# Performance work log

Hardware: AMD Instinct MI355X
Metric: run time of the kernel (lower is better)

The kernel has to match this reference:

```python
import jax, jax.numpy as jnp
import numpy as np

B, S, L, H, C = 16, 2048, 256, 768, 512

def setup_inputs() -> dict:
    key = jax.random.key(0)
    ks = jax.random.split(key, 9)
    sc = 1.0 / np.sqrt(H)
    return {
        "input_hidden_states": jax.random.normal(ks[0], (B, S, H), jnp.float32),
        "label_hidden_states": jax.random.normal(ks[1], (L, H), jnp.float32),
        "Wi": jax.random.normal(ks[2], (C, H), jnp.float32) * sc,
        "bi": jnp.zeros((C,), jnp.float32),
        "Wl": jax.random.normal(ks[3], (C, H), jnp.float32) * sc,
        "bl": jnp.zeros((C,), jnp.float32),
        "Wia": jax.random.normal(ks[4], (C, H), jnp.float32) * sc,
        "bia": jnp.zeros((C,), jnp.float32),
        "Wla": jax.random.normal(ks[5], (C, H), jnp.float32) * sc,
        "bla": jnp.zeros((C,), jnp.float32),
        "context": jax.random.uniform(ks[6], (C,), jnp.float32),
        "Wp": jax.random.normal(ks[7], (H, C), jnp.float32) * (1.0 / np.sqrt(C)),
    }

def reference(input_hidden_states, label_hidden_states, Wi, bi, Wl, bl,
              Wia, bia, Wla, bla, context, Wp):
    # Dropout is identity in eval mode.
    x = input_hidden_states            # [B,S,H]
    lab = label_hidden_states          # [L,H] (original repeats over batch; math is identical)
    input_trans = jax.nn.sigmoid(jnp.einsum('bsh,ch->bsc', x, Wi) + bi)      # [B,S,C]
    label_trans = jax.nn.sigmoid(lab @ Wl.T + bl)                            # [L,C]
    input_attn = jax.nn.sigmoid(jnp.einsum('bsh,ch->bsc', x, Wia) + bia)    # [B,S,C]
    label_attn = jax.nn.sigmoid(lab @ Wla.T + bla)                          # [L,C]
    # attn logits: (context * input_attn) @ label_attn^T  -> [B,S,L]
    logits = jnp.einsum('bsc,lc->bsl', input_attn * context, label_attn)
    attn = jax.nn.softmax(logits, axis=-1)                                   # [B,S,L]
    # trilinear reduction: sum_{s,l} input_trans[b,s,c] * attn[b,s,l] * label_trans[l,c]
    weighted = jnp.einsum('bsl,lc->bsc', attn, label_trans)                  # [B,S,C]
    fusion = jnp.sum(input_trans * weighted, axis=1)                         # [B,C]
    return fusion @ Wp.T                                                     # [B,H]
```

## Files before the change

### kernel.cpp

```cpp
#include <hip/hip_runtime.h>

#define H_DIM 768
#define C_DIM 512
#define L_DIM 256
#define S_DIM 2048
#define B_DIM 16

#define IA_STRIDE 520
#define ATTN_STRIDE 264

typedef __attribute__((ext_vector_type(8))) short short8;
typedef __attribute__((ext_vector_type(4))) float f32x4;
typedef __attribute__((ext_vector_type(2))) __fp16 half2v;

#define MFMA_F16(a, b, c) __builtin_amdgcn_mfma_f32_16x16x32_f16((a), (b), (c), 0, 0, 0)

__device__ __forceinline__ unsigned short f2h(float f) {
    _Float16 h = (_Float16)f;
    return __builtin_bit_cast(unsigned short, h);
}
__device__ __forceinline__ float h2f(unsigned short u) {
    _Float16 h = __builtin_bit_cast(_Float16, u);
    return (float)h;
}
__device__ __forceinline__ float sigmoid_f(float x) { return 1.0f / (1.0f + __expf(-x)); }

__device__ __forceinline__ short8 cvt8(const float* p) {
    const float4* q = (const float4*)(const void*)p;
    float4 u = q[0], v = q[1];
    half2v h0 = __builtin_amdgcn_cvt_pkrtz(u.x, u.y);
    half2v h1 = __builtin_amdgcn_cvt_pkrtz(u.z, u.w);
    half2v h2 = __builtin_amdgcn_cvt_pkrtz(v.x, v.y);
    half2v h3 = __builtin_amdgcn_cvt_pkrtz(v.z, v.w);
    int4 pk = { __builtin_bit_cast(int, h0), __builtin_bit_cast(int, h1),
                __builtin_bit_cast(int, h2), __builtin_bit_cast(int, h3) };
    return __builtin_bit_cast(short8, pk);
}


__global__ __launch_bounds__(256) void prep_w(
    const float* __restrict__ Wi, const float* __restrict__ Wia,
    const float* __restrict__ Wl, const float* __restrict__ Wla,
    unsigned short* __restrict__ Wi_f, unsigned short* __restrict__ Wia_f,
    unsigned short* __restrict__ Wl_f, unsigned short* __restrict__ Wla_f)
{
    const int tid = blockIdx.x * 256 + threadIdx.x;
    const int m   = tid / 49152;
    const int idx = tid - m * 49152;
    const int ct   = idx / 1536;
    const int rem  = idx - ct * 1536;
    const int kt   = rem >> 6;
    const int lane = rem & 63;
    const int row  = ct * 16 + (lane & 15);
    const int kcol = kt * 32 + (lane >> 4) * 8;
    const float* src = (m == 0 ? Wi : (m == 1 ? Wia : (m == 2 ? Wl : Wla)));
    unsigned short* dst = (m == 0 ? Wi_f : (m == 1 ? Wia_f : (m == 2 ? Wl_f : Wla_f)));
    short8 v = cvt8(src + (size_t)row * H_DIM + kcol);
    const int frag = ((ct >> 3) * 24 + kt) * 8 + (ct & 7);
    *(short8*)(void*)(dst + ((size_t)frag * 64 + lane) * 8) = v;
}

__global__ __launch_bounds__(256) void prep_x(
    const float* __restrict__ x, unsigned short* __restrict__ x_f)
{
    const int tid = blockIdx.x * 256 + threadIdx.x;
    const int mt  = tid / 1536;
    const int rem = tid - mt * 1536;
    const int kt  = rem >> 6;
    const int lane = rem & 63;
    const int row = mt * 16 + (lane & 15);
    const int col = kt * 32 + (lane >> 4) * 8;
    short8 v = cvt8(x + (size_t)row * H_DIM + col);
    *(short8*)(void*)(x_f + ((size_t)(mt * 24 + kt) * 64 + lane) * 8) = v;
}

__global__ __launch_bounds__(256) void label_mfma(
    const float* __restrict__ lab,
    const unsigned short* __restrict__ Wl_f,  const float* __restrict__ bl,
    const unsigned short* __restrict__ Wla_f, const float* __restrict__ bla,
    const float* __restrict__ ctx,
    unsigned short* __restrict__ la_f,
    unsigned short* __restrict__ lt_f)
{
    const int tid  = threadIdx.x;
    const int wave = tid >> 6;
    const int lane = tid & 63;
    const int quad = lane >> 4;
    const int c16  = lane & 15;
    const int ct2  = blockIdx.x & 7;
    const int mh   = blockIdx.x >> 3;
    const int ct   = ct2 * 4 + wave;
    const int n0   = ct * 16;
    const int l0   = mh * 32;

    const f32x4 z4 = {0.f, 0.f, 0.f, 0.f};
    f32x4 a1[2], a2[2];
#pragma unroll
    for (int mt = 0; mt < 2; ++mt) { a1[mt] = z4; a2[mt] = z4; }

    const float* lb = lab + (size_t)(l0 + c16) * H_DIM + quad * 8;
    const short8* wl8  = (const short8*)(const void*)Wl_f  + ((size_t)(ct >> 3) * 24 * 8 + (ct & 7)) * 64 + lane;
    const short8* wla8 = (const short8*)(const void*)Wla_f + ((size_t)(ct >> 3) * 24 * 8 + (ct & 7)) * 64 + lane;
    for (int kt = 0; kt < 24; ++kt) {
        short8 b1 = wl8[kt * 8 * 64];
        short8 b2 = wla8[kt * 8 * 64];
#pragma unroll
        for (int mt = 0; mt < 2; ++mt) {
            short8 a = cvt8(lb + mt * 16 * H_DIM + kt * 32);
            a1[mt] = MFMA_F16(a, b1, a1[mt]);
            a2[mt] = MFMA_F16(a, b2, a2[mt]);
        }
    }
    const int c = n0 + c16;
    const float blv = bl[c], blav = bla[c], cv = ctx[c];
#pragma unroll
    for (int mt = 0; mt < 2; ++mt)
#pragma unroll
        for (int r = 0; r < 4; ++r) {
            const int l = l0 + mt * 16 + quad * 4 + r;
            const float ltv = sigmoid_f(a1[mt][r] + blv);
            const float lav = sigmoid_f(a2[mt][r] + blav) * cv;
            {
                const int ctc = c >> 4, ktl = l >> 5;
                const int frag = ((ctc >> 3) * 8 + ktl) * 8 + (ctc & 7);
                const int ln = (c & 15) | (((l >> 3) & 3) << 4);
                lt_f[((size_t)frag * 64 + ln) * 8 + (l & 7)] = f2h(ltv);
            }
            {
                const int lt = l >> 4, ktc = c >> 5;
                const int frag = ((lt >> 2) * 16 + ktc) * 4 + (lt & 3);
                const int ln = (l & 15) | (((c >> 3) & 3) << 4);
                la_f[((size_t)frag * 64 + ln) * 8 + (c & 7)] = f2h(lav);
            }
        }
}

template<bool XF>
__global__ __launch_bounds__(256, 4) void fused_main(
    const unsigned short* __restrict__ x_f,
    const float* __restrict__ x,
    const float* __restrict__ bi,
    const float* __restrict__ bia,
    const unsigned short* __restrict__ Wi_f,
    const unsigned short* __restrict__ Wia_f,
    const unsigned short* __restrict__ lt_f,
    const unsigned short* __restrict__ la_f,
    float* __restrict__ fusion)
{
    __shared__ unsigned short lds_buf[32 * IA_STRIDE];
    __shared__ float rowscratch[4 * 32];
    __shared__ float inv_lds[32];

    const int tid  = threadIdx.x;
    const int wave = tid >> 6;
    const int lane = tid & 63;
    const int quad = lane >> 4;
    const int c16  = lane & 15;

    const int row0 = blockIdx.x * 32;
    const int b    = row0 >> 11;

    const f32x4 z4 = {0.f, 0.f, 0.f, 0.f};
    const int n0 = wave * 128;

    const float*  xb  = x + (size_t)(row0 + c16) * H_DIM + quad * 8;
    const short8* xf8 = (const short8*)(const void*)x_f + ((size_t)blockIdx.x * 2 * 24) * 64 + lane;

    {
        f32x4 acc[2][8];
#pragma unroll
        for (int mt = 0; mt < 2; ++mt)
#pragma unroll
            for (int nt = 0; nt < 8; ++nt) acc[mt][nt] = z4;
        const short8* wa8 = (const short8*)(const void*)Wia_f + (size_t)wave * 192 * 64 + lane;
        for (int kt = 0; kt < 24; ++kt) {
            short8 a0, a1;
            if constexpr (XF) { a0 = xf8[kt * 64]; a1 = xf8[(24 + kt) * 64]; }
            else { a0 = cvt8(xb + kt * 32); a1 = cvt8(xb + 16 * H_DIM + kt * 32); }
#pragma unroll
            for (int nt = 0; nt < 8; ++nt) {
                short8 ba = wa8[(kt * 8 + nt) * 64];
                acc[0][nt] = MFMA_F16(a0, ba, acc[0][nt]);
                acc[1][nt] = MFMA_F16(a1, ba, acc[1][nt]);
            }
        }
#pragma unroll
        for (int nt = 0; nt < 8; ++nt) {
            const int col = n0 + nt * 16 + c16;
            const float bv = bia[col];
#pragma unroll
            for (int mt = 0; mt < 2; ++mt)
#pragma unroll
                for (int r = 0; r < 4; ++r) {
                    const int row = mt * 16 + quad * 4 + r;
                    lds_buf[row * IA_STRIDE + col] = f2h(sigmoid_f(acc[mt][nt][r] + bv));
                }
        }
    }
    __syncthreads();

    const int n0l = wave * 64;
    f32x4 accl[2][4];
#pragma unroll
    for (int mt = 0; mt < 2; ++mt)
#pragma unroll
        for (int nt = 0; nt < 4; ++nt) accl[mt][nt] = z4;
    {
        const unsigned short* ab = lds_buf + c16 * IA_STRIDE + quad * 8;
        const short8* la8 = (const short8*)(const void*)la_f + (size_t)wave * 64 * 64 + lane;
        for (int kt = 0; kt < 16; ++kt) {
            const int kk = kt * 32;
            short8 a0 = *(const short8*)(const void*)(ab + kk);
            short8 a1 = *(const short8*)(const void*)(ab + 16 * IA_STRIDE + kk);
#pragma unroll
            for (int nt = 0; nt < 4; ++nt) {
                short8 bfr = la8[(kt * 4 + nt) * 64];
                accl[0][nt] = MFMA_F16(a0, bfr, accl[0][nt]);
                accl[1][nt] = MFMA_F16(a1, bfr, accl[1][nt]);
            }
        }
    }
    __syncthreads();

    float rmax[2][4];
#pragma unroll
    for (int mt = 0; mt < 2; ++mt)
#pragma unroll
        for (int r = 0; r < 4; ++r) {
            float m = accl[mt][0][r];
#pragma unroll
            for (int nt = 1; nt < 4; ++nt) m = fmaxf(m, accl[mt][nt][r]);
#pragma unroll
            for (int off = 1; off < 16; off <<= 1) m = fmaxf(m, __shfl_xor(m, off, 64));
            rmax[mt][r] = m;
        }
    if (c16 == 0) {
#pragma unroll
        for (int mt = 0; mt < 2; ++mt)
#pragma unroll
            for (int r = 0; r < 4; ++r)
                rowscratch[wave * 32 + mt * 16 + quad * 4 + r] = rmax[mt][r];
    }
    __syncthreads();
    float rsum[2][4];
#pragma unroll
    for (int mt = 0; mt < 2; ++mt)
#pragma unroll
        for (int r = 0; r < 4; ++r) {
            const int row = mt * 16 + quad * 4 + r;
            float gm = rowscratch[row];
#pragma unroll
            for (int w = 1; w < 4; ++w) gm = fmaxf(gm, rowscratch[w * 32 + row]);
            float s = 0.f;
#pragma unroll
            for (int nt = 0; nt < 4; ++nt) {
                float e = __expf(accl[mt][nt][r] - gm);
                accl[mt][nt][r] = e;
                s += e;
            }
#pragma unroll
            for (int off = 1; off < 16; off <<= 1) s += __shfl_xor(s, off, 64);
            rsum[mt][r] = s;
        }
    __syncthreads();
    if (c16 == 0) {
#pragma unroll
        for (int mt = 0; mt < 2; ++mt)
#pragma unroll
            for (int r = 0; r < 4; ++r)
                rowscratch[wave * 32 + mt * 16 + quad * 4 + r] = rsum[mt][r];
    }
    __syncthreads();
#pragma unroll
    for (int mt = 0; mt < 2; ++mt)
#pragma unroll
        for (int r = 0; r < 4; ++r) {
            const int row = mt * 16 + quad * 4 + r;
            const float st = rowscratch[row] + rowscratch[32 + row]
                           + rowscratch[64 + row] + rowscratch[96 + row];
            if (wave == 0 && c16 == 0) inv_lds[row] = 1.0f / st;
#pragma unroll
            for (int nt = 0; nt < 4; ++nt)
                lds_buf[row * ATTN_STRIDE + n0l + nt * 16 + c16] = f2h(accl[mt][nt][r]);
        }
    __syncthreads();

    f32x4 accw[2][8];
#pragma unroll
    for (int mt = 0; mt < 2; ++mt)
#pragma unroll
        for (int nt = 0; nt < 8; ++nt) accw[mt][nt] = z4;
    {
        const unsigned short* ab = lds_buf + c16 * ATTN_STRIDE + quad * 8;
        const short8* lt8 = (const short8*)(const void*)lt_f + (size_t)wave * 64 * 64 + lane;
        for (int kt = 0; kt < 8; ++kt) {
            const int kk = kt * 32;
            short8 a0 = *(const short8*)(const void*)(ab + kk);
            short8 a1 = *(const short8*)(const void*)(ab + 16 * ATTN_STRIDE + kk);
#pragma unroll
            for (int nt = 0; nt < 8; ++nt) {
                short8 bfr = lt8[(kt * 8 + nt) * 64];
                accw[0][nt] = MFMA_F16(a0, bfr, accw[0][nt]);
                accw[1][nt] = MFMA_F16(a1, bfr, accw[1][nt]);
            }
        }
    }
    __syncthreads();

    {
        float invr[2][4];
#pragma unroll
        for (int mt = 0; mt < 2; ++mt)
#pragma unroll
            for (int r = 0; r < 4; ++r) invr[mt][r] = inv_lds[mt * 16 + quad * 4 + r];
#pragma unroll
        for (int nt = 0; nt < 8; ++nt) {
            const int col = n0 + nt * 16 + c16;
#pragma unroll
            for (int mt = 0; mt < 2; ++mt)
#pragma unroll
                for (int r = 0; r < 4; ++r) {
                    const int row = mt * 16 + quad * 4 + r;
                    lds_buf[row * IA_STRIDE + col] = f2h(accw[mt][nt][r] * invr[mt][r]);
                }
        }
    }

    {
        f32x4 acc[2][8];
#pragma unroll
        for (int mt = 0; mt < 2; ++mt)
#pragma unroll
            for (int nt = 0; nt < 8; ++nt) acc[mt][nt] = z4;
        const short8* wi8 = (const short8*)(const void*)Wi_f + (size_t)wave * 192 * 64 + lane;
        for (int kt = 0; kt < 24; ++kt) {
            short8 a0, a1;
            if constexpr (XF) { a0 = xf8[kt * 64]; a1 = xf8[(24 + kt) * 64]; }
            else { a0 = cvt8(xb + kt * 32); a1 = cvt8(xb + 16 * H_DIM + kt * 32); }
#pragma unroll
            for (int nt = 0; nt < 8; ++nt) {
                short8 bw = wi8[(kt * 8 + nt) * 64];
                acc[0][nt] = MFMA_F16(a0, bw, acc[0][nt]);
                acc[1][nt] = MFMA_F16(a1, bw, acc[1][nt]);
            }
        }
#pragma unroll
        for (int nt = 0; nt < 8; ++nt) {
            const int col = n0 + nt * 16 + c16;
            const float bv = bi[col];
            float s = 0.f;
#pragma unroll
            for (int mt = 0; mt < 2; ++mt)
#pragma unroll
                for (int r = 0; r < 4; ++r) {
                    const int row = mt * 16 + quad * 4 + r;
                    s += h2f(lds_buf[row * IA_STRIDE + col]) * sigmoid_f(acc[mt][nt][r] + bv);
                }
            s += __shfl_xor(s, 16, 64);
            s += __shfl_xor(s, 32, 64);
            if (lane < 16) atomicAdd(&fusion[b * C_DIM + col], s);
        }
    }
}

__global__ __launch_bounds__(256) void out_kernel(
    const float* __restrict__ fusion,
    const float* __restrict__ Wp,
    float* __restrict__ out)
{
    const int idx = blockIdx.x * 256 + threadIdx.x;
    const int R   = idx >> 3;
    const int sub = idx & 7;
    const int bb  = R / H_DIM;
    const int h   = R - bb * H_DIM;
    const float* wp = Wp + (size_t)h * C_DIM;
    const float* f  = fusion + bb * C_DIM;
    float s = 0.f;
#pragma unroll
    for (int j = 0; j < 16; ++j) {
        const int c = j * 32 + sub * 4;
        float4 wv = *(const float4*)(const void*)(wp + c);
        float4 fv = *(const float4*)(const void*)(f + c);
        s += fv.x * wv.x + fv.y * wv.y + fv.z * wv.z + fv.w * wv.w;
    }
    s += __shfl_xor(s, 1, 64);
    s += __shfl_xor(s, 2, 64);
    s += __shfl_xor(s, 4, 64);
    if (sub == 0) out[R] = s;
}

extern "C" void kernel_launch(void* const* d_in, const int* in_sizes, int n_in,
                              void* d_out, int out_size, void* d_ws, size_t ws_size,
                              hipStream_t stream)
{
    const float* x    = (const float*)d_in[0];
    const float* lab  = (const float*)d_in[1];
    const float* Wi   = (const float*)d_in[2];
    const float* bi   = (const float*)d_in[3];
    const float* Wl   = (const float*)d_in[4];
    const float* bl   = (const float*)d_in[5];
    const float* Wia  = (const float*)d_in[6];
    const float* bia  = (const float*)d_in[7];
    const float* Wla  = (const float*)d_in[8];
    const float* bla  = (const float*)d_in[9];
    const float* ctx  = (const float*)d_in[10];
    const float* Wp   = (const float*)d_in[11];

    char* ws = (char*)d_ws;
    unsigned short* Wi_f  = (unsigned short*)(ws);
    unsigned short* Wia_f = (unsigned short*)(ws + 786432);
    unsigned short* Wl_f  = (unsigned short*)(ws + 1572864);
    unsigned short* Wla_f = (unsigned short*)(ws + 2359296);
    unsigned short* la_f  = (unsigned short*)(ws + 3145728);
    unsigned short* lt_f  = (unsigned short*)(ws + 3407872);
    float* fusion         = (float*)(ws + 3670016);
    unsigned short* x_f   = (unsigned short*)(ws + 3702784);
    const size_t NEED_XF  = 3702784 + (size_t)32768 * 768 * 2;

    (void)hipMemsetAsync(fusion, 0, B_DIM * C_DIM * sizeof(float), stream);
    prep_w<<<768, 256, 0, stream>>>(Wi, Wia, Wl, Wla, Wi_f, Wia_f, Wl_f, Wla_f);
    label_mfma<<<64, 256, 0, stream>>>(lab, Wl_f, bl, Wla_f, bla, ctx, la_f, lt_f);
    if (ws_size >= NEED_XF) {
        prep_x<<<12288, 256, 0, stream>>>(x, x_f);
        fused_main<true><<<(B_DIM * S_DIM) / 32, 256, 0, stream>>>(
            x_f, x, bi, bia, Wi_f, Wia_f, lt_f, la_f, fusion);
    } else {
        fused_main<false><<<(B_DIM * S_DIM) / 32, 256, 0, stream>>>(
            nullptr, x, bi, bia, Wi_f, Wia_f, lt_f, la_f, fusion);
    }
    out_kernel<<<384, 256, 0, stream>>>(fusion, Wp, (float*)d_out);
}
```

Measured before the change: 332.4 us.

## Enlarge fused block to 64 rows with 8 waves and 4x4 MFMA tiles

The fused main kernel now handles 64 rows per block with 512 threads (8 waves). Each wave owns a 4x4 grid of MFMA tiles instead of 2x8, which cuts how often each weight fragment is loaded per row and gives a squarer register tile. The fragment layouts for x, the weights and the label tensors are regrouped to match, and the label kernel is split into smaller tiles. The x and weight conversion kernels and the fusion zeroing are merged into one launch, replacing the memset and one kernel launch. The cost is a larger LDS footprint, more accumulator registers per wave and a cross-wave softmax reduction over 8 waves, all of which may reduce occupancy.

```diff
diff --git a/kernel.cpp b/kernel.cpp
--- a/kernel.cpp
+++ b/kernel.cpp
@@ -38,40 +38,48 @@
 }
 
 
-__global__ __launch_bounds__(256) void prep_w(
+__global__ __launch_bounds__(256) void prep_all(
+    const float* __restrict__ x,
     const float* __restrict__ Wi, const float* __restrict__ Wia,
     const float* __restrict__ Wl, const float* __restrict__ Wla,
+    unsigned short* __restrict__ x_f,
     unsigned short* __restrict__ Wi_f, unsigned short* __restrict__ Wia_f,
-    unsigned short* __restrict__ Wl_f, unsigned short* __restrict__ Wla_f)
+    unsigned short* __restrict__ Wl_f, unsigned short* __restrict__ Wla_f,
+    float* __restrict__ fusion, int nx)
 {
-    const int tid = blockIdx.x * 256 + threadIdx.x;
-    const int m   = tid / 49152;
-    const int idx = tid - m * 49152;
-    const int ct   = idx / 1536;
-    const int rem  = idx - ct * 1536;
-    const int kt   = rem >> 6;
-    const int lane = rem & 63;
-    const int row  = ct * 16 + (lane & 15);
-    const int kcol = kt * 32 + (lane >> 4) * 8;
-    const float* src = (m == 0 ? Wi : (m == 1 ? Wia : (m == 2 ? Wl : Wla)));
-    unsigned short* dst = (m == 0 ? Wi_f : (m == 1 ? Wia_f : (m == 2 ? Wl_f : Wla_f)));
-    short8 v = cvt8(src + (size_t)row * H_DIM + kcol);
-    const int frag = ((ct >> 3) * 24 + kt) * 8 + (ct & 7);
-    *(short8*)(void*)(dst + ((size_t)frag * 64 + lane) * 8) = v;
-}
-
-__global__ __launch_bounds__(256) void prep_x(
-    const float* __restrict__ x, unsigned short* __restrict__ x_f)
-{
-    const int tid = blockIdx.x * 256 + threadIdx.x;
-    const int mt  = tid / 1536;
-    const int rem = tid - mt * 1536;
-    const int kt  = rem >> 6;
-    const int lane = rem & 63;
-    const int row = mt * 16 + (lane & 15);
-    const int col = kt * 32 + (lane >> 4) * 8;
-    short8 v = cvt8(x + (size_t)row * H_DIM + col);
-    *(short8*)(void*)(x_f + ((size_t)(mt * 24 + kt) * 64 + lane) * 8) = v;
+    int bid = blockIdx.x;
+    if (bid < nx) {
+        const int tid = bid * 256 + threadIdx.x;
+        const int mt  = tid / 1536;
+        const int rem = tid - mt * 1536;
+        const int kt  = rem >> 6;
+        const int lane = rem & 63;
+        const int row = mt * 16 + (lane & 15);
+        const int col = kt * 32 + (lane >> 4) * 8;
+        short8 v = cvt8(x + (size_t)row * H_DIM + col);
+        const int frag = ((mt >> 2) * 24 + kt) * 4 + (mt & 3);
+        *(short8*)(void*)(x_f + ((size_t)frag * 64 + lane) * 8) = v;
+        return;
+    }
+    bid -= nx;
+    if (bid < 768) {
+        const int tid = bid * 256 + threadIdx.x;
+        const int m   = tid / 49152;
+        const int idx = tid - m * 49152;
+        const int ct   = idx / 1536;
+        const int rem  = idx - ct * 1536;
+        const int kt   = rem >> 6;
+        const int lane = rem & 63;
+        const int row  = ct * 16 + (lane & 15);
+        const int kcol = kt * 32 + (lane >> 4) * 8;
+        const float* src = (m == 0 ? Wi : (m == 1 ? Wia : (m == 2 ? Wl : Wla)));
+        unsigned short* dst = (m == 0 ? Wi_f : (m == 1 ? Wia_f : (m == 2 ? Wl_f : Wla_f)));
+        short8 v = cvt8(src + (size_t)row * H_DIM + kcol);
+        const int frag = ((ct >> 2) * 24 + kt) * 4 + (ct & 3);
+        *(short8*)(void*)(dst + ((size_t)frag * 64 + lane) * 8) = v;
+        return;
+    }
+    for (int i = threadIdx.x; i < B_DIM * C_DIM; i += 256) fusion[i] = 0.f;
 }
 
 __global__ __launch_bounds__(256) void label_mfma(
@@ -89,54 +97,46 @@
     const int c16  = lane & 15;
     const int ct2  = blockIdx.x & 7;
     const int mh   = blockIdx.x >> 3;
-    const int ct   = ct2 * 4 + wave;
-    const int n0   = ct * 16;
-    const int l0   = mh * 32;
+    const int n0   = (ct2 * 4 + wave) * 16;
+    const int l0   = mh * 16;
 
     const f32x4 z4 = {0.f, 0.f, 0.f, 0.f};
-    f32x4 a1[2], a2[2];
-#pragma unroll
-    for (int mt = 0; mt < 2; ++mt) { a1[mt] = z4; a2[mt] = z4; }
+    f32x4 a1 = z4, a2 = z4;
 
     const float* lb = lab + (size_t)(l0 + c16) * H_DIM + quad * 8;
-    const short8* wl8  = (const short8*)(const void*)Wl_f  + ((size_t)(ct >> 3) * 24 * 8 + (ct & 7)) * 64 + lane;
-    const short8* wla8 = (const short8*)(const void*)Wla_f + ((size_t)(ct >> 3) * 24 * 8 + (ct & 7)) * 64 + lane;
+    const short8* wl8  = (const short8*)(const void*)Wl_f  + ((size_t)ct2 * 96 + wave) * 64 + lane;
+    const short8* wla8 = (const short8*)(const void*)Wla_f + ((size_t)ct2 * 96 + wave) * 64 + lane;
     for (int kt = 0; kt < 24; ++kt) {
-        short8 b1 = wl8[kt * 8 * 64];
-        short8 b2 = wla8[kt * 8 * 64];
-#pragma unroll
-        for (int mt = 0; mt < 2; ++mt) {
-            short8 a = cvt8(lb + mt * 16 * H_DIM + kt * 32);
-            a1[mt] = MFMA_F16(a, b1, a1[mt]);
-            a2[mt] = MFMA_F16(a, b2, a2[mt]);
-        }
+        short8 b1 = wl8[kt * 4 * 64];
+        short8 b2 = wla8[kt * 4 * 64];
+        short8 a  = cvt8(lb + kt * 32);
+        a1 = MFMA_F16(a, b1, a1);
+        a2 = MFMA_F16(a, b2, a2);
     }
     const int c = n0 + c16;
     const float blv = bl[c], blav = bla[c], cv = ctx[c];
 #pragma unroll
-    for (int mt = 0; mt < 2; ++mt)
-#pragma unroll
-        for (int r = 0; r < 4; ++r) {
-            const int l = l0 + mt * 16 + quad * 4 + r;
-            const float ltv = sigmoid_f(a1[mt][r] + blv);
-            const float lav = sigmoid_f(a2[mt][r] + blav) * cv;
-            {
-                const int ctc = c >> 4, ktl = l >> 5;
-                const int frag = ((ctc >> 3) * 8 + ktl) * 8 + (ctc & 7);
-                const int ln = (c & 15) | (((l >> 3) & 3) << 4);
-                lt_f[((size_t)frag * 64 + ln) * 8 + (l & 7)] = f2h(ltv);
-            }
-            {
-                const int lt = l >> 4, ktc = c >> 5;
-                const int frag = ((lt >> 2) * 16 + ktc) * 4 + (lt & 3);
-                const int ln = (l & 15) | (((c >> 3) & 3) << 4);
-                la_f[((size_t)frag * 64 + ln) * 8 + (c & 7)] = f2h(lav);
-            }
-        }
+    for (int r = 0; r < 4; ++r) {
+        const int l = l0 + quad * 4 + r;
+        const float ltv = sigmoid_f(a1[r] + blv);
+        const float lav = sigmoid_f(a2[r] + blav) * cv;
+        {
+            const int ctc = c >> 4, ktl = l >> 5;
+            const int frag = ((ctc >> 2) * 8 + ktl) * 4 + (ctc & 3);
+            const int ln = (c & 15) | (((l >> 3) & 3) << 4);
+            lt_f[((size_t)frag * 64 + ln) * 8 + (l & 7)] = f2h(ltv);
+        }
+        {
+            const int lt = l >> 4, ktc = c >> 5;
+            const int frag = ((lt >> 1) * 16 + ktc) * 2 + (lt & 1);
+            const int ln = (l & 15) | (((c >> 3) & 3) << 4);
+            la_f[((size_t)frag * 64 + ln) * 8 + (c & 7)] = f2h(lav);
+        }
+    }
 }
 
 template<bool XF>
-__global__ __launch_bounds__(256, 4) void fused_main(
+__global__ __launch_bounds__(512, 4) void fused_main(
     const unsigned short* __restrict__ x_f,
     const float* __restrict__ x,
     const float* __restrict__ bi,
@@ -147,9 +147,9 @@
     const unsigned short* __restrict__ la_f,
     float* __restrict__ fusion)
 {
-    __shared__ unsigned short lds_buf[32 * IA_STRIDE];
-    __shared__ float rowscratch[4 * 32];
-    __shared__ float inv_lds[32];
+    __shared__ unsigned short lds_buf[64 * IA_STRIDE];
+    __shared__ float rowscratch[8 * 64];
+    __shared__ float inv_lds[64];
 
     const int tid  = threadIdx.x;
     const int wave = tid >> 6;
@@ -157,204 +157,208 @@
     const int quad = lane >> 4;
     const int c16  = lane & 15;
 
-    const int row0 = blockIdx.x * 32;
+    const int row0 = blockIdx.x * 64;
     const int b    = row0 >> 11;
 
     const f32x4 z4 = {0.f, 0.f, 0.f, 0.f};
-    const int n0 = wave * 128;
+    const int n0  = wave * 64;
+    const int n0l = wave * 32;
 
     const float*  xb  = x + (size_t)(row0 + c16) * H_DIM + quad * 8;
-    const short8* xf8 = (const short8*)(const void*)x_f + ((size_t)blockIdx.x * 2 * 24) * 64 + lane;
+    const short8* xf8 = (const short8*)(const void*)x_f + ((size_t)blockIdx.x * 96) * 64 + lane;
 
     {
-        f32x4 acc[2][8];
-#pragma unroll
-        for (int mt = 0; mt < 2; ++mt)
-#pragma unroll
-            for (int nt = 0; nt < 8; ++nt) acc[mt][nt] = z4;
-        const short8* wa8 = (const short8*)(const void*)Wia_f + (size_t)wave * 192 * 64 + lane;
+        f32x4 acc[4][4];
+#pragma unroll
+        for (int m = 0; m < 4; ++m)
+#pragma unroll
+            for (int p = 0; p < 4; ++p) acc[m][p] = z4;
+        const short8* wa8 = (const short8*)(const void*)Wia_f + ((size_t)wave * 96) * 64 + lane;
         for (int kt = 0; kt < 24; ++kt) {
-            short8 a0, a1;
-            if constexpr (XF) { a0 = xf8[kt * 64]; a1 = xf8[(24 + kt) * 64]; }
-            else { a0 = cvt8(xb + kt * 32); a1 = cvt8(xb + 16 * H_DIM + kt * 32); }
-#pragma unroll
-            for (int nt = 0; nt < 8; ++nt) {
-                short8 ba = wa8[(kt * 8 + nt) * 64];
-                acc[0][nt] = MFMA_F16(a0, ba, acc[0][nt]);
-                acc[1][nt] = MFMA_F16(a1, ba, acc[1][nt]);
+            short8 a[4], bw[4];
+#pragma unroll
+            for (int m = 0; m < 4; ++m) {
+                if constexpr (XF) a[m] = xf8[(kt * 4 + m) * 64];
+                else a[m] = cvt8(xb + m * 16 * H_DIM + kt * 32);
             }
-        }
-#pragma unroll
-        for (int nt = 0; nt < 8; ++nt) {
-            const int col = n0 + nt * 16 + c16;
+#pragma unroll
+            for (int p = 0; p < 4; ++p) bw[p] = wa8[(kt * 4 + p) * 64];
+#pragma unroll
+            for (int m = 0; m < 4; ++m)
+#pragma unroll
+                for (int p = 0; p < 4; ++p) acc[m][p] = MFMA_F16(a[m], bw[p], acc[m][p]);
+        }
+#pragma unroll
+        for (int p = 0; p < 4; ++p) {
+            const int col = n0 + p * 16 + c16;
             const float bv = bia[col];
 #pragma unroll
-            for (int mt = 0; mt < 2; ++mt)
+            for (int m = 0; m < 4; ++m)
 #pragma unroll
                 for (int r = 0; r < 4; ++r) {
-                    const int row = mt * 16 + quad * 4 + r;
-                    lds_buf[row * IA_STRIDE + col] = f2h(sigmoid_f(acc[mt][nt][r] + bv));
+                    const int row = m * 16 + quad * 4 + r;
+                    lds_buf[row * IA_STRIDE + col] = f2h(sigmoid_f(acc[m][p][r] + bv));
                 }
         }
     }
     __syncthreads();
 
-    const int n0l = wave * 64;
-    f32x4 accl[2][4];
-#pragma unroll
-    for (int mt = 0; mt < 2; ++mt)
-#pragma unroll
-        for (int nt = 0; nt < 4; ++nt) accl[mt][nt] = z4;
+    f32x4 accl[4][2];
+#pragma unroll
+    for (int m = 0; m < 4; ++m) { accl[m][0] = z4; accl[m][1] = z4; }
     {
         const unsigned short* ab = lds_buf + c16 * IA_STRIDE + quad * 8;
-        const short8* la8 = (const short8*)(const void*)la_f + (size_t)wave * 64 * 64 + lane;
+        const short8* la8 = (const short8*)(const void*)la_f + ((size_t)wave * 32) * 64 + lane;
         for (int kt = 0; kt < 16; ++kt) {
             const int kk = kt * 32;
-            short8 a0 = *(const short8*)(const void*)(ab + kk);
-            short8 a1 = *(const short8*)(const void*)(ab + 16 * IA_STRIDE + kk);
-#pragma unroll
-            for (int nt = 0; nt < 4; ++nt) {
-                short8 bfr = la8[(kt * 4 + nt) * 64];
-                accl[0][nt] = MFMA_F16(a0, bfr, accl[0][nt]);
-                accl[1][nt] = MFMA_F16(a1, bfr, accl[1][nt]);
+            short8 a[4], bq[2];
+#pragma unroll
+            for (int m = 0; m < 4; ++m)
+                a[m] = *(const short8*)(const void*)(ab + m * 16 * IA_STRIDE + kk);
+            bq[0] = la8[(kt * 2 + 0) * 64];
+            bq[1] = la8[(kt * 2 + 1) * 64];
+#pragma unroll
+            for (int m = 0; m < 4; ++m) {
+                accl[m][0] = MFMA_F16(a[m], bq[0], accl[m][0]);
+                accl[m][1] = MFMA_F16(a[m], bq[1], accl[m][1]);
             }
         }
     }
     __syncthreads();
 
-    float rmax[2][4];
-#pragma unroll
-    for (int mt = 0; mt < 2; ++mt)
+    float rmax[4][4];
+#pragma unroll
+    for (int m = 0; m < 4; ++m)
 #pragma unroll
         for (int r = 0; r < 4; ++r) {
-            float m = accl[mt][0][r];
-#pragma unroll
-            for (int nt = 1; nt < 4; ++nt) m = fmaxf(m, accl[mt][nt][r]);
-#pragma unroll
-            for (int off = 1; off < 16; off <<= 1) m = fmaxf(m, __shfl_xor(m, off, 64));
-            rmax[mt][r] = m;
+            float mm = fmaxf(accl[m][0][r], accl[m][1][r]);
+#pragma unroll
+            for (int off = 1; off < 16; off <<= 1) mm = fmaxf(mm, __shfl_xor(mm, off, 64));
+            rmax[m][r] = mm;
         }
     if (c16 == 0) {
 #pragma unroll
-        for (int mt = 0; mt < 2; ++mt)
+        for (int m = 0; m < 4; ++m)
 #pragma unroll
             for (int r = 0; r < 4; ++r)
-                rowscratch[wave * 32 + mt * 16 + quad * 4 + r] = rmax[mt][r];
-    }
-    __syncthreads();
-    float rsum[2][4];
-#pragma unroll
-    for (int mt = 0; mt < 2; ++mt)
+                rowscratch[wave * 64 + m * 16 + quad * 4 + r] = rmax[m][r];
+    }
+    __syncthreads();
+    float rsum[4][4];
+#pragma unroll
+    for (int m = 0; m < 4; ++m)
 #pragma unroll
         for (int r = 0; r < 4; ++r) {
-            const int row = mt * 16 + quad * 4 + r;
+            const int row = m * 16 + quad * 4 + r;
             float gm = rowscratch[row];
 #pragma unroll
-            for (int w = 1; w < 4; ++w) gm = fmaxf(gm, rowscratch[w * 32 + row]);
-            float s = 0.f;
-#pragma unroll
-            for (int nt = 0; nt < 4; ++nt) {
-                float e = __expf(accl[mt][nt][r] - gm);
-                accl[mt][nt][r] = e;
-                s += e;
-            }
+            for (int w = 1; w < 8; ++w) gm = fmaxf(gm, rowscratch[w * 64 + row]);
+            float e0 = __expf(accl[m][0][r] - gm);
+            float e1 = __expf(accl[m][1][r] - gm);
+            accl[m][0][r] = e0; accl[m][1][r] = e1;
+            float s = e0 + e1;
 #pragma unroll
             for (int off = 1; off < 16; off <<= 1) s += __shfl_xor(s, off, 64);
-            rsum[mt][r] = s;
+            rsum[m][r] = s;
         }
     __syncthreads();
     if (c16 == 0) {
 #pragma unroll
-        for (int mt = 0; mt < 2; ++mt)
+        for (int m = 0; m < 4; ++m)
 #pragma unroll
             for (int r = 0; r < 4; ++r)
-                rowscratch[wave * 32 + mt * 16 + quad * 4 + r] = rsum[mt][r];
-    }
-    __syncthreads();
-#pragma unroll
-    for (int mt = 0; mt < 2; ++mt)
+                rowscratch[wave * 64 + m * 16 + quad * 4 + r] = rsum[m][r];
+    }
+    __syncthreads();
+#pragma unroll
+    for (int m = 0; m < 4; ++m)
 #pragma unroll
         for (int r = 0; r < 4; ++r) {
-            const int row = mt * 16 + quad * 4 + r;
-            const float st = rowscratch[row] + rowscratch[32 + row]
-                           + rowscratch[64 + row] + rowscratch[96 + row];
+            const int row = m * 16 + quad * 4 + r;
+            float st = rowscratch[row];
+#pragma unroll
+            for (int w = 1; w < 8; ++w) st += rowscratch[w * 64 + row];
             if (wave == 0 && c16 == 0) inv_lds[row] = 1.0f / st;
-#pragma unroll
-            for (int nt = 0; nt < 4; ++nt)
-                lds_buf[row * ATTN_STRIDE + n0l + nt * 16 + c16] = f2h(accl[mt][nt][r]);
-        }
-    __syncthreads();
-
-    f32x4 accw[2][8];
-#pragma unroll
-    for (int mt = 0; mt < 2; ++mt)
-#pragma unroll
-        for (int nt = 0; nt < 8; ++nt) accw[mt][nt] = z4;
+            lds_buf[row * ATTN_STRIDE + n0l + 0 * 16 + c16] = f2h(accl[m][0][r]);
+            lds_buf[row * ATTN_STRIDE + n0l + 1 * 16 + c16] = f2h(accl[m][1][r]);
+        }
+    __syncthreads();
+
+    f32x4 accw[4][4];
+#pragma unroll
+    for (int m = 0; m < 4; ++m)
+#pragma unroll
+        for (int p = 0; p < 4; ++p) accw[m][p] = z4;
     {
         const unsigned short* ab = lds_buf + c16 * ATTN_STRIDE + quad * 8;
-        const short8* lt8 = (const short8*)(const void*)lt_f + (size_t)wave * 64 * 64 + lane;
+        const short8* lt8 = (const short8*)(const void*)lt_f + ((size_t)wave * 32) * 64 + lane;
         for (int kt = 0; kt < 8; ++kt) {
             const int kk = kt * 32;
-            short8 a0 = *(const short8*)(const void*)(ab + kk);
-            short8 a1 = *(const short8*)(const void*)(ab + 16 * ATTN_STRIDE + kk);
-#pragma unroll
-            for (int nt = 0; nt < 8; ++nt) {
-                short8 bfr = lt8[(kt * 8 + nt) * 64];
-                accw[0][nt] = MFMA_F16(a0, bfr, accw[0][nt]);
-                accw[1][nt] = MFMA_F16(a1, bfr, accw[1][nt]);
+            short8 a[4], bp[4];
+#pragma unroll
+            for (int m = 0; m < 4; ++m)
+                a[m] = *(const short8*)(const void*)(ab + m * 16 * ATTN_STRIDE + kk);
+#pragma unroll
+            for (int p = 0; p < 4; ++p) bp[p] = lt8[(kt * 4 + p) * 64];
+#pragma unroll
+            for (int m = 0; m < 4; ++m)
+#pragma unroll
+                for (int p = 0; p < 4; ++p) accw[m][p] = MFMA_F16(a[m], bp[p], accw[m][p]);
+        }
+    }
+    __syncthreads();
+
+    {
+        float invr[4][4];
+#pragma unroll
+        for (int m = 0; m < 4; ++m)
+#pragma unroll
+            for (int r = 0; r < 4; ++r) invr[m][r] = inv_lds[m * 16 + quad * 4 + r];
+#pragma unroll
+        for (int p = 0; p < 4; ++p) {
+            const int col = n0 + p * 16 + c16;
+#pragma unroll
+            for (int m = 0; m < 4; ++m)
+#pragma unroll
+                for (int r = 0; r < 4; ++r) {
+                    const int row = m * 16 + quad * 4 + r;
+                    lds_buf[row * IA_STRIDE + col] = f2h(accw[m][p][r] * invr[m][r]);
+                }
+        }
+    }
+
+    {
+        f32x4 acc[4][4];
+#pragma unroll
+        for (int m = 0; m < 4; ++m)
+#pragma unroll
+            for (int p = 0; p < 4; ++p) acc[m][p] = z4;
+        const short8* wi8 = (const short8*)(const void*)Wi_f + ((size_t)wave * 96) * 64 + lane;
+        for (int kt = 0; kt < 24; ++kt) {
+            short8 a[4], bw[4];
+#pragma unroll
+            for (int m = 0; m < 4; ++m) {
+                if constexpr (XF) a[m] = xf8[(kt * 4 + m) * 64];
+                else a[m] = cvt8(xb + m * 16 * H_DIM + kt * 32);
             }
-        }
-    }
-    __syncthreads();
-
-    {
-        float invr[2][4];
-#pragma unroll
-        for (int mt = 0; mt < 2; ++mt)
-#pragma unroll
-            for (int r = 0; r < 4; ++r) invr[mt][r] = inv_lds[mt * 16 + quad * 4 + r];
-#pragma unroll
-        for (int nt = 0; nt < 8; ++nt) {
-            const int col = n0 + nt * 16 + c16;
-#pragma unroll
-            for (int mt = 0; mt < 2; ++mt)
-#pragma unroll
-                for (int r = 0; r < 4; ++r) {
-                    const int row = mt * 16 + quad * 4 + r;
-                    lds_buf[row * IA_STRIDE + col] = f2h(accw[mt][nt][r] * invr[mt][r]);
-                }
-        }
-    }
-
-    {
-        f32x4 acc[2][8];
-#pragma unroll
-        for (int mt = 0; mt < 2; ++mt)
-#pragma unroll
-            for (int nt = 0; nt < 8; ++nt) acc[mt][nt] = z4;
-        const short8* wi8 = (const short8*)(const void*)Wi_f + (size_t)wave * 192 * 64 + lane;
-        for (int kt = 0; kt < 24; ++kt) {
-            short8 a0, a1;
-            if constexpr (XF) { a0 = xf8[kt * 64]; a1 = xf8[(24 + kt) * 64]; }
-            else { a0 = cvt8(xb + kt * 32); a1 = cvt8(xb + 16 * H_DIM + kt * 32); }
-#pragma unroll
-            for (int nt = 0; nt < 8; ++nt) {
-                short8 bw = wi8[(kt * 8 + nt) * 64];
-                acc[0][nt] = MFMA_F16(a0, bw, acc[0][nt]);
-                acc[1][nt] = MFMA_F16(a1, bw, acc[1][nt]);
-            }
-        }
-#pragma unroll
-        for (int nt = 0; nt < 8; ++nt) {
-            const int col = n0 + nt * 16 + c16;
+#pragma unroll
+            for (int p = 0; p < 4; ++p) bw[p] = wi8[(kt * 4 + p) * 64];
+#pragma unroll
+            for (int m = 0; m < 4; ++m)
+#pragma unroll
+                for (int p = 0; p < 4; ++p) acc[m][p] = MFMA_F16(a[m], bw[p], acc[m][p]);
+        }
+#pragma unroll
+        for (int p = 0; p < 4; ++p) {
+            const int col = n0 + p * 16 + c16;
             const float bv = bi[col];
             float s = 0.f;
 #pragma unroll
-            for (int mt = 0; mt < 2; ++mt)
+            for (int m = 0; m < 4; ++m)
 #pragma unroll
                 for (int r = 0; r < 4; ++r) {
-                    const int row = mt * 16 + quad * 4 + r;
-                    s += h2f(lds_buf[row * IA_STRIDE + col]) * sigmoid_f(acc[mt][nt][r] + bv);
+                    const int row = m * 16 + quad * 4 + r;
+                    s += h2f(lds_buf[row * IA_STRIDE + col]) * sigmoid_f(acc[m][p][r] + bv);
                 }
             s += __shfl_xor(s, 16, 64);
             s += __shfl_xor(s, 32, 64);
@@ -417,15 +421,16 @@
     unsigned short* x_f   = (unsigned short*)(ws + 3702784);
     const size_t NEED_XF  = 3702784 + (size_t)32768 * 768 * 2;
 
-    (void)hipMemsetAsync(fusion, 0, B_DIM * C_DIM * sizeof(float), stream);
-    prep_w<<<768, 256, 0, stream>>>(Wi, Wia, Wl, Wla, Wi_f, Wia_f, Wl_f, Wla_f);
-    label_mfma<<<64, 256, 0, stream>>>(lab, Wl_f, bl, Wla_f, bla, ctx, la_f, lt_f);
-    if (ws_size >= NEED_XF) {
-        prep_x<<<12288, 256, 0, stream>>>(x, x_f);
-        fused_main<true><<<(B_DIM * S_DIM) / 32, 256, 0, stream>>>(
+    const bool xf = (ws_size >= NEED_XF);
+    const int nx = xf ? 12288 : 0;
+    prep_all<<<nx + 769, 256, 0, stream>>>(x, Wi, Wia, Wl, Wla,
+                                           x_f, Wi_f, Wia_f, Wl_f, Wla_f, fusion, nx);
+    label_mfma<<<128, 256, 0, stream>>>(lab, Wl_f, bl, Wla_f, bla, ctx, la_f, lt_f);
+    if (xf) {
+        fused_main<true><<<(B_DIM * S_DIM) / 64, 512, 0, stream>>>(
             x_f, x, bi, bia, Wi_f, Wia_f, lt_f, la_f, fusion);
     } else {
-        fused_main<false><<<(B_DIM * S_DIM) / 32, 256, 0, stream>>>(
+        fused_main<false><<<(B_DIM * S_DIM) / 64, 512, 0, stream>>>(
             nullptr, x, bi, bia, Wi_f, Wia_f, lt_f, la_f, fusion);
     }
     out_kernel<<<384, 256, 0, stream>>>(fusion, Wp, (float*)d_out);
```

After: 380.3 us. +14.4%, slower.

## Merge weight, input and label preprocessing plus memset into one launch

Applied to the files above, without the earlier changes.

Replaces the memset, prep_w, label_mfma and prep_x launches with a single prep_all kernel whose block ranges handle the label projection, the x conversion, the Wi/Wia conversion and the fusion zeroing. The label projection now reads and converts fp32 Wl/Wla directly, so the fragment-packed copies of those two weights are no longer produced. This removes three launch boundaries and the serial dependency between weight prep and the label GEMM. In exchange the label blocks do redundant fp32 conversions and the kernel branches heavily by block index.

```diff
diff --git a/kernel.cpp b/kernel.cpp
--- a/kernel.cpp
+++ b/kernel.cpp
@@ -38,88 +38,49 @@
 }
 
 
-__global__ __launch_bounds__(256) void prep_w(
+__global__ __launch_bounds__(256) void prep_all(
+    const float* __restrict__ x,
     const float* __restrict__ Wi, const float* __restrict__ Wia,
-    const float* __restrict__ Wl, const float* __restrict__ Wla,
+    const float* __restrict__ lab,
+    const float* __restrict__ Wl,  const float* __restrict__ bl,
+    const float* __restrict__ Wla, const float* __restrict__ bla,
+    const float* __restrict__ ctx,
+    unsigned short* __restrict__ x_f,
     unsigned short* __restrict__ Wi_f, unsigned short* __restrict__ Wia_f,
-    unsigned short* __restrict__ Wl_f, unsigned short* __restrict__ Wla_f)
+    unsigned short* __restrict__ la_f, unsigned short* __restrict__ lt_f,
+    float* __restrict__ fusion, int nx)
 {
-    const int tid = blockIdx.x * 256 + threadIdx.x;
-    const int m   = tid / 49152;
-    const int idx = tid - m * 49152;
-    const int ct   = idx / 1536;
-    const int rem  = idx - ct * 1536;
-    const int kt   = rem >> 6;
-    const int lane = rem & 63;
-    const int row  = ct * 16 + (lane & 15);
-    const int kcol = kt * 32 + (lane >> 4) * 8;
-    const float* src = (m == 0 ? Wi : (m == 1 ? Wia : (m == 2 ? Wl : Wla)));
-    unsigned short* dst = (m == 0 ? Wi_f : (m == 1 ? Wia_f : (m == 2 ? Wl_f : Wla_f)));
-    short8 v = cvt8(src + (size_t)row * H_DIM + kcol);
-    const int frag = ((ct >> 3) * 24 + kt) * 8 + (ct & 7);
-    *(short8*)(void*)(dst + ((size_t)frag * 64 + lane) * 8) = v;
-}
-
-__global__ __launch_bounds__(256) void prep_x(
-    const float* __restrict__ x, unsigned short* __restrict__ x_f)
-{
-    const int tid = blockIdx.x * 256 + threadIdx.x;
-    const int mt  = tid / 1536;
-    const int rem = tid - mt * 1536;
-    const int kt  = rem >> 6;
-    const int lane = rem & 63;
-    const int row = mt * 16 + (lane & 15);
-    const int col = kt * 32 + (lane >> 4) * 8;
-    short8 v = cvt8(x + (size_t)row * H_DIM + col);
-    *(short8*)(void*)(x_f + ((size_t)(mt * 24 + kt) * 64 + lane) * 8) = v;
-}
-
-__global__ __launch_bounds__(256) void label_mfma(
-    const float* __restrict__ lab,
-    const unsigned short* __restrict__ Wl_f,  const float* __restrict__ bl,
-    const unsigned short* __restrict__ Wla_f, const float* __restrict__ bla,
-    const float* __restrict__ ctx,
-    unsigned short* __restrict__ la_f,
-    unsigned short* __restrict__ lt_f)
-{
-    const int tid  = threadIdx.x;
-    const int wave = tid >> 6;
-    const int lane = tid & 63;
-    const int quad = lane >> 4;
-    const int c16  = lane & 15;
-    const int ct2  = blockIdx.x & 7;
-    const int mh   = blockIdx.x >> 3;
-    const int ct   = ct2 * 4 + wave;
-    const int n0   = ct * 16;
-    const int l0   = mh * 32;
-
-    const f32x4 z4 = {0.f, 0.f, 0.f, 0.f};
-    f32x4 a1[2], a2[2];
-#pragma unroll
-    for (int mt = 0; mt < 2; ++mt) { a1[mt] = z4; a2[mt] = z4; }
-
-    const float* lb = lab + (size_t)(l0 + c16) * H_DIM + quad * 8;
-    const short8* wl8  = (const short8*)(const void*)Wl_f  + ((size_t)(ct >> 3) * 24 * 8 + (ct & 7)) * 64 + lane;
-    const short8* wla8 = (const short8*)(const void*)Wla_f + ((size_t)(ct >> 3) * 24 * 8 + (ct & 7)) * 64 + lane;
-    for (int kt = 0; kt < 24; ++kt) {
-        short8 b1 = wl8[kt * 8 * 64];
-        short8 b2 = wla8[kt * 8 * 64];
-#pragma unroll
-        for (int mt = 0; mt < 2; ++mt) {
-            short8 a = cvt8(lb + mt * 16 * H_DIM + kt * 32);
-            a1[mt] = MFMA_F16(a, b1, a1[mt]);
-            a2[mt] = MFMA_F16(a, b2, a2[mt]);
-        }
-    }
-    const int c = n0 + c16;
-    const float blv = bl[c], blav = bla[c], cv = ctx[c];
-#pragma unroll
-    for (int mt = 0; mt < 2; ++mt)
+    int bid = blockIdx.x;
+    if (bid < 128) {
+        const int tid  = threadIdx.x;
+        const int wave = tid >> 6;
+        const int lane = tid & 63;
+        const int quad = lane >> 4;
+        const int c16  = lane & 15;
+        const int ct2  = bid & 7;
+        const int mh   = bid >> 3;
+        const int n0   = (ct2 * 4 + wave) * 16;
+        const int l0   = mh * 16;
+
+        const f32x4 z4 = {0.f, 0.f, 0.f, 0.f};
+        f32x4 a1 = z4, a2 = z4;
+        const float* lb  = lab + (size_t)(l0 + c16) * H_DIM + quad * 8;
+        const float* wl  = Wl  + (size_t)(n0 + c16) * H_DIM + quad * 8;
+        const float* wla = Wla + (size_t)(n0 + c16) * H_DIM + quad * 8;
+        for (int kt = 0; kt < 24; ++kt) {
+            short8 b1 = cvt8(wl + kt * 32);
+            short8 b2 = cvt8(wla + kt * 32);
+            short8 a  = cvt8(lb + kt * 32);
+            a1 = MFMA_F16(a, b1, a1);
+            a2 = MFMA_F16(a, b2, a2);
+        }
+        const int c = n0 + c16;
+        const float blv = bl[c], blav = bla[c], cv = ctx[c];
 #pragma unroll
         for (int r = 0; r < 4; ++r) {
-            const int l = l0 + mt * 16 + quad * 4 + r;
-            const float ltv = sigmoid_f(a1[mt][r] + blv);
-            const float lav = sigmoid_f(a2[mt][r] + blav) * cv;
+            const int l = l0 + quad * 4 + r;
+            const float ltv = sigmoid_f(a1[r] + blv);
+            const float lav = sigmoid_f(a2[r] + blav) * cv;
             {
                 const int ctc = c >> 4, ktl = l >> 5;
                 const int frag = ((ctc >> 3) * 8 + ktl) * 8 + (ctc & 7);
@@ -133,6 +94,40 @@
                 la_f[((size_t)frag * 64 + ln) * 8 + (c & 7)] = f2h(lav);
             }
         }
+        return;
+    }
+    bid -= 128;
+    if (bid < nx) {
+        const int tid = bid * 256 + threadIdx.x;
+        const int mt  = tid / 1536;
+        const int rem = tid - mt * 1536;
+        const int kt  = rem >> 6;
+        const int lane = rem & 63;
+        const int row = mt * 16 + (lane & 15);
+        const int col = kt * 32 + (lane >> 4) * 8;
+        short8 v = cvt8(x + (size_t)row * H_DIM + col);
+        *(short8*)(void*)(x_f + ((size_t)(mt * 24 + kt) * 64 + lane) * 8) = v;
+        return;
+    }
+    bid -= nx;
+    if (bid < 384) {
+        const int tid = bid * 256 + threadIdx.x;
+        const int m   = tid / 49152;
+        const int idx = tid - m * 49152;
+        const int ct   = idx / 1536;
+        const int rem  = idx - ct * 1536;
+        const int kt   = rem >> 6;
+        const int lane = rem & 63;
+        const int row  = ct * 16 + (lane & 15);
+        const int kcol = kt * 32 + (lane >> 4) * 8;
+        const float* src = (m == 0 ? Wi : Wia);
+        unsigned short* dst = (m == 0 ? Wi_f : Wia_f);
+        short8 v = cvt8(src + (size_t)row * H_DIM + kcol);
+        const int frag = ((ct >> 3) * 24 + kt) * 8 + (ct & 7);
+        *(short8*)(void*)(dst + ((size_t)frag * 64 + lane) * 8) = v;
+        return;
+    }
+    for (int i = threadIdx.x; i < B_DIM * C_DIM; i += 256) fusion[i] = 0.f;
 }
 
 template<bool XF>
@@ -409,19 +404,18 @@
     char* ws = (char*)d_ws;
     unsigned short* Wi_f  = (unsigned short*)(ws);
     unsigned short* Wia_f = (unsigned short*)(ws + 786432);
-    unsigned short* Wl_f  = (unsigned short*)(ws + 1572864);
-    unsigned short* Wla_f = (unsigned short*)(ws + 2359296);
-    unsigned short* la_f  = (unsigned short*)(ws + 3145728);
-    unsigned short* lt_f  = (unsigned short*)(ws + 3407872);
-    float* fusion         = (float*)(ws + 3670016);
-    unsigned short* x_f   = (unsigned short*)(ws + 3702784);
-    const size_t NEED_XF  = 3702784 + (size_t)32768 * 768 * 2;
-
-    (void)hipMemsetAsync(fusion, 0, B_DIM * C_DIM * sizeof(float), stream);
-    prep_w<<<768, 256, 0, stream>>>(Wi, Wia, Wl, Wla, Wi_f, Wia_f, Wl_f, Wla_f);
-    label_mfma<<<64, 256, 0, stream>>>(lab, Wl_f, bl, Wla_f, bla, ctx, la_f, lt_f);
-    if (ws_size >= NEED_XF) {
-        prep_x<<<12288, 256, 0, stream>>>(x, x_f);
+    unsigned short* la_f  = (unsigned short*)(ws + 1572864);
+    unsigned short* lt_f  = (unsigned short*)(ws + 1835008);
+    float* fusion         = (float*)(ws + 2097152);
+    unsigned short* x_f   = (unsigned short*)(ws + 2129920);
+    const size_t NEED_XF  = 2129920 + (size_t)32768 * 768 * 2;
+
+    const bool xf = (ws_size >= NEED_XF);
+    const int nx = xf ? 12288 : 0;
+    prep_all<<<128 + nx + 384 + 1, 256, 0, stream>>>(
+        x, Wi, Wia, lab, Wl, bl, Wla, bla, ctx,
+        x_f, Wi_f, Wia_f, la_f, lt_f, fusion, nx);
+    if (xf) {
         fused_main<true><<<(B_DIM * S_DIM) / 32, 256, 0, stream>>>(
             x_f, x, bi, bia, Wi_f, Wia_f, lt_f, la_f, fusion);
     } else {
```

Measured after the change: 338.9 us. Within noise of the previous version (+2.0%).
